# Kernel tuning notes

Hardware: AMD Instinct MI355X
Metric: run time of the kernel (lower is better)

Reference implementation:

```python
import jax, jax.numpy as jnp
import numpy as np

EPS = 1e-05


def setup_inputs() -> dict:
    key = jax.random.key(0)
    kx, kw, kb, kg, kp, kq = jax.random.split(key, 6)
    B, S, D = 32, 1024, 1024
    x = jax.random.normal(kx, (B, S, D), dtype=jnp.float32)
    # Linear(input_size, input_size) params
    W = jax.random.normal(kw, (D, D), dtype=jnp.float32) / np.sqrt(D)
    b = jax.random.normal(kb, (D,), dtype=jnp.float32) * 0.01
    gold_opinion = jax.random.uniform(kg, (B, S, 5), dtype=jnp.float32)
    predict_opinion = jax.random.uniform(kp, (B, S, 5), dtype=jnp.float32)
    gold_prob = jax.random.uniform(kq, (), dtype=jnp.float32)
    return {"x": x, "W": W, "b": b, "gold_opinion": gold_opinion,
            "predict_opinion": predict_opinion, "gold_prob": gold_prob}


def reference(x, W, b, gold_opinion, predict_opinion, gold_prob):
    # x: [B, S, D]
    S = x.shape[-2]
    x_tran = jnp.einsum('bsd,ed->bse', x, W) + b           # Linear: x @ W^T + b
    weights = jnp.einsum('bsd,btd->bst', x_tran, x)        # QK^T -> [B, S, S]

    idx = jnp.arange(S)
    location = jnp.abs(idx[None, :] - idx[:, None]).astype(x.dtype)  # [S, S]
    weights = weights * (1.0 / (location + EPS))           # distance decay

    # use_opinion = True branch
    gold_op = gold_opinion[:, :, 1] + gold_opinion[:, :, 2]          # [B, S]
    pred_op = predict_opinion[:, :, 3] + predict_opinion[:, :, 4]    # [B, S]
    opinion_weights = gold_prob * gold_op + (1.0 - gold_prob) * pred_op
    weights = weights * opinion_weights[:, :, None]

    weights = jnp.exp(jnp.tanh(weights))                   # pseudo-softmax numerator
    off_diag = (location != 0).astype(weights.dtype)       # eye(S) == 0 mask
    weights = weights * off_diag
    weights = weights / (jnp.sum(weights, axis=-1, keepdims=True) + EPS)
    return jnp.einsum('bst,btd->bsd', weights, x)
```

## Files before the change

kernel.cpp:

```cpp
#include <hip/hip_runtime.h>

#define EPSF 1e-5f

typedef _Float16 f16x8 __attribute__((ext_vector_type(8)));
typedef float f32x4 __attribute__((ext_vector_type(4)));

__device__ __forceinline__ void gload_lds16(const _Float16* g, _Float16* l) {
  __builtin_amdgcn_global_load_lds(
      (const __attribute__((address_space(1))) unsigned int*)g,
      (__attribute__((address_space(3))) unsigned int*)l, 16, 0, 0);
}

__device__ __forceinline__ f16x8 cvt8(float4 a, float4 b) {
  f16x8 h;
  h[0] = (_Float16)a.x; h[1] = (_Float16)a.y; h[2] = (_Float16)a.z; h[3] = (_Float16)a.w;
  h[4] = (_Float16)b.x; h[5] = (_Float16)b.y; h[6] = (_Float16)b.z; h[7] = (_Float16)b.w;
  return h;
}

__device__ __forceinline__ void gemm256_run(const _Float16* __restrict__ Ag,
                                            const _Float16* __restrict__ Bg,
                                            _Float16* lds, f32x4 (&acc)[8][4]) {
  const int tid = threadIdx.x;
  const int wave = tid >> 6, lane = tid & 63;
  const int wm = wave >> 2, wn = wave & 3;
  const int quad = lane >> 4, nl = lane & 15;
  const int swz = nl & 7;
  const long stg_off = (long)(wave * 8 + (lane >> 3)) * 1024 +
                       (((lane & 7) ^ (lane >> 3)) * 8);

#pragma unroll
  for (int i = 0; i < 8; ++i)
#pragma unroll
    for (int j = 0; j < 4; ++j) acc[i][j] = (f32x4){0.f, 0.f, 0.f, 0.f};

  f16x8 af[4], bf[4];

#define STG(G, T1, q, isB)                                                   \
  gload_lds16((G) + (long)(q) * 65536 + stg_off + (T1) * 64,                 \
              lds + (((T1) & 1) * 32768 + (isB) * 16384 + (q) * 4096 + wave * 512))
#define LDB4(bb, ksub)                                                       \
  {                                                                          \
    const _Float16* pB_ = lds + (bb) * 32768 + 16384 + (wn * 64 + nl) * 64 + \
                          ((((ksub) * 4 + quad) ^ swz) * 8);                 \
    _Pragma("unroll") for (int j_ = 0; j_ < 4; ++j_)                         \
        bf[j_] = *(const f16x8*)(pB_ + j_ * 1024);                           \
  }
#define LDA4(bb, mq, ksub)                                                   \
  {                                                                          \
    const _Float16* pA_ = lds + (bb) * 32768 +                               \
                          (wm * 128 + (mq) * 64 + nl) * 64 +                 \
                          ((((ksub) * 4 + quad) ^ swz) * 8);                 \
    _Pragma("unroll") for (int i_ = 0; i_ < 4; ++i_)                         \
        af[i_] = *(const f16x8*)(pA_ + i_ * 1024);                           \
  }
#define MFMA16(mq)                                                           \
  {                                                                          \
    __builtin_amdgcn_s_setprio(1);                                           \
    _Pragma("unroll") for (int i_ = 0; i_ < 4; ++i_)                         \
        _Pragma("unroll") for (int j_ = 0; j_ < 4; ++j_)                     \
            acc[(mq) * 4 + i_][j_] = __builtin_amdgcn_mfma_f32_16x16x32_f16( \
                af[i_], bf[j_], acc[(mq) * 4 + i_][j_], 0, 0, 0);            \
    __builtin_amdgcn_s_setprio(0);                                           \
  }
#define BAR __builtin_amdgcn_s_barrier()
#define LGKM0 asm volatile("s_waitcnt lgkmcnt(0)" ::: "memory")
#define VMW2 asm volatile("s_waitcnt vmcnt(2)" ::: "memory")
#define VMW0 asm volatile("s_waitcnt vmcnt(0)" ::: "memory")

  STG(Bg, 0, 0, 1); STG(Bg, 0, 1, 1);
  STG(Ag, 0, 0, 0); STG(Ag, 0, 2, 0);
  STG(Bg, 0, 2, 1); STG(Bg, 0, 3, 1);
  STG(Ag, 0, 1, 0); STG(Ag, 0, 3, 0);
  VMW2;
  BAR;

#pragma unroll 2
  for (int T = 0; T < 15; ++T) {
    const int bb = T & 1;
    LDB4(bb, 0); LDA4(bb, 0, 0);
    STG(Bg, T + 1, 0, 1); STG(Bg, T + 1, 1, 1);
    BAR; LGKM0; MFMA16(0); VMW2; BAR;
    LDA4(bb, 1, 0);
    STG(Ag, T + 1, 0, 0); STG(Ag, T + 1, 2, 0);
    BAR; LGKM0; MFMA16(1); BAR;
    LDB4(bb, 1); LDA4(bb, 0, 1);
    STG(Bg, T + 1, 2, 1); STG(Bg, T + 1, 3, 1);
    BAR; LGKM0; MFMA16(0); BAR;
    LDA4(bb, 1, 1);
    STG(Ag, T + 1, 1, 0); STG(Ag, T + 1, 3, 0);
    BAR; LGKM0; MFMA16(1); VMW2; BAR;
  }
  {
    LDB4(1, 0); LDA4(1, 0, 0);
    BAR; LGKM0; MFMA16(0); VMW0; BAR;
    LDA4(1, 1, 0);
    BAR; LGKM0; MFMA16(1); BAR;
    LDB4(1, 1); LDA4(1, 0, 1);
    BAR; LGKM0; MFMA16(0); BAR;
    LDA4(1, 1, 1);
    BAR; LGKM0; MFMA16(1); BAR;
  }
#undef VMW0
#undef VMW2
#undef LGKM0
#undef BAR
#undef MFMA16
#undef LDA4
#undef LDB4
#undef STG
}

__global__ void prep_opin_k(const float* __restrict__ gold, const float* __restrict__ pred,
                            const float* __restrict__ gprob, float* __restrict__ opin, int n) {
  int i = blockIdx.x * 256 + threadIdx.x;
  if (i >= n) return;
  float gp = gprob[0];
  float go = gold[i * 5 + 1] + gold[i * 5 + 2];
  float po = pred[i * 5 + 3] + pred[i * 5 + 4];
  opin[i] = gp * go + (1.0f - gp) * po;
}

__global__ __launch_bounds__(256) void prep_h_k(const float* __restrict__ src,
                                                _Float16* __restrict__ dst) {
  long i = ((long)blockIdx.x * 256 + threadIdx.x) * 8;
  float4 a = *(const float4*)(src + i);
  float4 b = *(const float4*)(src + i + 4);
  *(f16x8*)(dst + i) = cvt8(a, b);
}

__global__ __launch_bounds__(256) void prep_xt_k(const float* __restrict__ x,
                                                 _Float16* __restrict__ XhT) {
  __shared__ _Float16 T[64][66];
  const int d0 = blockIdx.x * 64, t0 = blockIdx.y * 64;
  const long base = (long)blockIdx.z * 1024;
  const int c = threadIdx.x & 63, tr = threadIdx.x >> 6;
#pragma unroll
  for (int k = 0; k < 16; ++k) {
    int t = k * 4 + tr;
    T[t][c] = (_Float16)x[(base + t0 + t) * 1024 + d0 + c];
  }
  __syncthreads();
#pragma unroll
  for (int k = 0; k < 16; ++k) {
    int d = k * 4 + tr;
    XhT[(base + d0 + d) * 1024 + t0 + c] = T[c][d];
  }
}

__global__ __launch_bounds__(512, 2) void gemm12_k(const _Float16* __restrict__ Xh,
                                                   const _Float16* __restrict__ Wh,
                                                   const float* __restrict__ bias,
                                                   _Float16* __restrict__ XT) {
  __shared__ _Float16 lds[2 * 32768];
  const int lin = blockIdx.x;
  const int ii = lin >> 3;
  const int mt = (lin & 7) * 16 + (ii >> 2);
  const int nt = ii & 3;
  const long m0 = (long)mt * 256;
  const int n0 = nt * 256;

  f32x4 acc[8][4];
  gemm256_run(Xh + m0 * 1024, Wh + (long)n0 * 1024, lds, acc);

  const int tid = threadIdx.x;
  const int wave = tid >> 6, lane = tid & 63;
  const int wm = wave >> 2, wn = wave & 3;
  const int quad = lane >> 4, nl = lane & 15;
#pragma unroll
  for (int mi = 0; mi < 8; ++mi) {
    long gm = m0 + wm * 128 + mi * 16 + quad * 4;
#pragma unroll
    for (int ni = 0; ni < 4; ++ni) {
      int gn = n0 + wn * 64 + ni * 16 + nl;
      float bv = bias[gn];
#pragma unroll
      for (int r = 0; r < 4; ++r)
        XT[(gm + r) * 1024 + gn] = (_Float16)(acc[mi][ni][r] + bv);
    }
  }
}

__global__ __launch_bounds__(512, 2) void scores2_k(const _Float16* __restrict__ XT,
                                                    const _Float16* __restrict__ Xh,
                                                    const float* __restrict__ opin,
                                                    _Float16* __restrict__ P,
                                                    float* __restrict__ denom) {
  __shared__ _Float16 lds[2 * 32768];
  const int lin = blockIdx.x;
  const int ii = lin >> 3;
  const int b = (lin & 7) + 8 * (ii >> 4);
  const int tile = ii & 15;
  const int s0 = (tile >> 2) * 256;
  const int t0 = (tile & 3) * 256;
  const long base = (long)b * 1024;

  f32x4 acc[8][4];
  gemm256_run(XT + (base + s0) * 1024, Xh + (base + t0) * 1024, lds, acc);

  const int tid = threadIdx.x;
  const int wave = tid >> 6, lane = tid & 63;
  const int wm = wave >> 2, wn = wave & 3;
  const int quad = lane >> 4, nl = lane & 15;
#pragma unroll
  for (int mi = 0; mi < 8; ++mi) {
#pragma unroll
    for (int r = 0; r < 4; ++r) {
      int s = s0 + wm * 128 + mi * 16 + quad * 4 + r;
      float opv = opin[b * 1024 + s];
      float rs = 0.f;
#pragma unroll
      for (int ni = 0; ni < 4; ++ni) {
        int tc = t0 + wn * 64 + ni * 16 + nl;
        float loc = fabsf((float)(s - tc));
        float arg = acc[mi][ni][r] * (1.0f / (loc + EPSF)) * opv;
        float th = 1.f - 2.f / (__expf(2.f * arg) + 1.f);
        float p = __expf(th);
        if (s == tc) p = 0.f;
        P[(base + s) * 1024 + tc] = (_Float16)p;
        rs += p;
      }
      rs += __shfl_xor(rs, 1);
      rs += __shfl_xor(rs, 2);
      rs += __shfl_xor(rs, 4);
      rs += __shfl_xor(rs, 8);
      if (nl == 0) atomicAdd(&denom[b * 1024 + s], rs);
    }
  }
}

__global__ __launch_bounds__(512, 2) void pv2_k(const _Float16* __restrict__ P,
                                                const _Float16* __restrict__ XhT,
                                                const float* __restrict__ denom,
                                                float* __restrict__ out) {
  __shared__ _Float16 lds[2 * 32768];
  const int lin = blockIdx.x;
  const int ii = lin >> 3;
  const int b = (lin & 7) + 8 * (ii >> 4);
  const int tile = ii & 15;
  const int s0 = (tile >> 2) * 256;
  const int d0 = (tile & 3) * 256;
  const long base = (long)b * 1024;

  f32x4 acc[8][4];
  gemm256_run(P + (base + s0) * 1024, XhT + (base + d0) * 1024, lds, acc);

  const int tid = threadIdx.x;
  const int wave = tid >> 6, lane = tid & 63;
  const int wm = wave >> 2, wn = wave & 3;
  const int quad = lane >> 4, nl = lane & 15;
#pragma unroll
  for (int mi = 0; mi < 8; ++mi) {
#pragma unroll
    for (int r = 0; r < 4; ++r) {
      int s = s0 + wm * 128 + mi * 16 + quad * 4 + r;
      float inv = 1.0f / (denom[b * 1024 + s] + EPSF);
#pragma unroll
      for (int ni = 0; ni < 4; ++ni) {
        int d = d0 + wn * 64 + ni * 16 + nl;
        out[(base + s) * 1024 + d] = acc[mi][ni][r] * inv;
      }
    }
  }
}

__global__ __launch_bounds__(256) void gemm1_k(const _Float16* __restrict__ Xh,
                                               const float* __restrict__ Wt,
                                               const float* __restrict__ bias,
                                               _Float16* __restrict__ XT) {
  __shared__ _Float16 As[128 * 32];
  __shared__ _Float16 Bs[128 * 32];
  const int tid = threadIdx.x;
  const int wave = tid >> 6, lane = tid & 63;
  const int wm = wave >> 1, wn = wave & 1;
  const int quad = lane >> 4, nl = lane & 15;
  const long m0 = (long)blockIdx.y * 128;
  const int n0 = blockIdx.x * 128;

  f32x4 acc[4][4];
  f32x4 zero = {0.f, 0.f, 0.f, 0.f};
#pragma unroll
  for (int i = 0; i < 4; ++i)
#pragma unroll
    for (int j = 0; j < 4; ++j) acc[i][j] = zero;

  const int crow = tid >> 2;
  const int ckc = (tid & 3) * 8;

  for (int k0 = 0; k0 < 1024; k0 += 32) {
#pragma unroll
    for (int it = 0; it < 2; ++it) {
      int c = it * 256 + tid;
      gload_lds16(Xh + (m0 + (c >> 2)) * 1024 + k0 + (c & 3) * 8,
                  &As[(it * 256 + wave * 64) * 8]);
      int row = it * 64 + crow;
      const float* sb = Wt + (long)(n0 + row) * 1024 + k0 + ckc;
      float4 b0 = *(const float4*)sb;
      float4 b1 = *(const float4*)(sb + 4);
      *(f16x8*)&Bs[row * 32 + ckc] = cvt8(b0, b1);
    }
    __syncthreads();
    f16x8 af[4], bf[4];
#pragma unroll
    for (int mi = 0; mi < 4; ++mi)
      af[mi] = *(const f16x8*)&As[(wm * 64 + mi * 16 + nl) * 32 + quad * 8];
#pragma unroll
    for (int ni = 0; ni < 4; ++ni)
      bf[ni] = *(const f16x8*)&Bs[(wn * 64 + ni * 16 + nl) * 32 + quad * 8];
#pragma unroll
    for (int mi = 0; mi < 4; ++mi)
#pragma unroll
      for (int ni = 0; ni < 4; ++ni)
        acc[mi][ni] = __builtin_amdgcn_mfma_f32_16x16x32_f16(af[mi], bf[ni], acc[mi][ni], 0, 0, 0);
    __syncthreads();
  }

#pragma unroll
  for (int mi = 0; mi < 4; ++mi) {
    long gm = m0 + wm * 64 + mi * 16 + quad * 4;
#pragma unroll
    for (int ni = 0; ni < 4; ++ni) {
      int gn = n0 + wn * 64 + ni * 16 + nl;
      float bv = bias[gn];
#pragma unroll
      for (int r = 0; r < 4; ++r)
        XT[(gm + r) * 1024 + gn] = (_Float16)(acc[mi][ni][r] + bv);
    }
  }
}

__global__ __launch_bounds__(256) void scores_f_k(const _Float16* __restrict__ XT,
                                                  const _Float16* __restrict__ Xh,
                                                  const float* __restrict__ opin,
                                                  _Float16* __restrict__ P,
                                                  float* __restrict__ denom) {
  __shared__ _Float16 As[128 * 32];
  __shared__ _Float16 Bs[128 * 32];
  const int tid = threadIdx.x;
  const int wave = tid >> 6, lane = tid & 63;
  const int wm = wave >> 1, wn = wave & 1;
  const int quad = lane >> 4, nl = lane & 15;
  const int b = blockIdx.z;
  const int s0 = blockIdx.y * 128;
  const int t0 = blockIdx.x * 128;
  const long base = (long)b * 1024;

  f32x4 acc[4][4];
  f32x4 zero = {0.f, 0.f, 0.f, 0.f};
#pragma unroll
  for (int i = 0; i < 4; ++i)
#pragma unroll
    for (int j = 0; j < 4; ++j) acc[i][j] = zero;

  for (int k0 = 0; k0 < 1024; k0 += 32) {
#pragma unroll
    for (int it = 0; it < 2; ++it) {
      int c = it * 256 + tid;
      gload_lds16(XT + (base + s0 + (c >> 2)) * 1024 + k0 + (c & 3) * 8,
                  &As[(it * 256 + wave * 64) * 8]);
      gload_lds16(Xh + (base + t0 + (c >> 2)) * 1024 + k0 + (c & 3) * 8,
                  &Bs[(it * 256 + wave * 64) * 8]);
    }
    __syncthreads();
    f16x8 af[4], bf[4];
#pragma unroll
    for (int mi = 0; mi < 4; ++mi)
      af[mi] = *(const f16x8*)&As[(wm * 64 + mi * 16 + nl) * 32 + quad * 8];
#pragma unroll
    for (int ni = 0; ni < 4; ++ni)
      bf[ni] = *(const f16x8*)&Bs[(wn * 64 + ni * 16 + nl) * 32 + quad * 8];
#pragma unroll
    for (int mi = 0; mi < 4; ++mi)
#pragma unroll
      for (int ni = 0; ni < 4; ++ni)
        acc[mi][ni] = __builtin_amdgcn_mfma_f32_16x16x32_f16(af[mi], bf[ni], acc[mi][ni], 0, 0, 0);
    __syncthreads();
  }

#pragma unroll
  for (int mi = 0; mi < 4; ++mi) {
#pragma unroll
    for (int r = 0; r < 4; ++r) {
      int s = s0 + wm * 64 + mi * 16 + quad * 4 + r;
      float opv = opin[b * 1024 + s];
      float rs = 0.f;
#pragma unroll
      for (int ni = 0; ni < 4; ++ni) {
        int t = t0 + wn * 64 + ni * 16 + nl;
        float loc = fabsf((float)(s - t));
        float arg = acc[mi][ni][r] * (1.0f / (loc + EPSF)) * opv;
        float th = 1.f - 2.f / (__expf(2.f * arg) + 1.f);
        float p = __expf(th);
        if (s == t) p = 0.f;
        P[(base + s) * 1024 + t] = (_Float16)p;
        rs += p;
      }
      rs += __shfl_xor(rs, 1);
      rs += __shfl_xor(rs, 2);
      rs += __shfl_xor(rs, 4);
      rs += __shfl_xor(rs, 8);
      if (nl == 0) atomicAdd(&denom[b * 1024 + s], rs);
    }
  }
}

__global__ __launch_bounds__(256) void pv_k(const _Float16* __restrict__ P,
                                            const float* __restrict__ X,
                                            const float* __restrict__ denom,
                                            float* __restrict__ out) {
  __shared__ _Float16 As[128 * 32];
  __shared__ _Float16 BsT[128 * 40];
  const int tid = threadIdx.x;
  const int wave = tid >> 6, lane = tid & 63;
  const int wm = wave >> 1, wn = wave & 1;
  const int quad = lane >> 4, nl = lane & 15;
  const int b = blockIdx.z;
  const int s0 = blockIdx.y * 128;
  const int d0 = blockIdx.x * 128;
  const long base = (long)b * 1024;

  const int dcol = tid & 127;
  const int tg = tid >> 7;

  f32x4 acc[4][4];
  f32x4 zero = {0.f, 0.f, 0.f, 0.f};
#pragma unroll
  for (int i = 0; i < 4; ++i)
#pragma unroll
    for (int j = 0; j < 4; ++j) acc[i][j] = zero;

  for (int k0 = 0; k0 < 1024; k0 += 32) {
#pragma unroll
    for (int it = 0; it < 2; ++it) {
      int c = it * 256 + tid;
      gload_lds16(P + (base + s0 + (c >> 2)) * 1024 + k0 + (c & 3) * 8,
                  &As[(it * 256 + wave * 64) * 8]);
    }
    {
      const float* xb = X + (base + k0 + tg * 16) * 1024 + d0 + dcol;
      float v[16];
#pragma unroll
      for (int j = 0; j < 16; ++j) v[j] = xb[j * 1024];
      f16x8 h0, h1;
#pragma unroll
      for (int j = 0; j < 8; ++j) { h0[j] = (_Float16)v[j]; h1[j] = (_Float16)v[8 + j]; }
      *(f16x8*)&BsT[dcol * 40 + tg * 16] = h0;
      *(f16x8*)&BsT[dcol * 40 + tg * 16 + 8] = h1;
    }
    __syncthreads();
    f16x8 af[4], bf[4];
#pragma unroll
    for (int mi = 0; mi < 4; ++mi)
      af[mi] = *(const f16x8*)&As[(wm * 64 + mi * 16 + nl) * 32 + quad * 8];
#pragma unroll
    for (int ni = 0; ni < 4; ++ni)
      bf[ni] = *(const f16x8*)&BsT[(wn * 64 + ni * 16 + nl) * 40 + quad * 8];
#pragma unroll
    for (int mi = 0; mi < 4; ++mi)
#pragma unroll
      for (int ni = 0; ni < 4; ++ni)
        acc[mi][ni] = __builtin_amdgcn_mfma_f32_16x16x32_f16(af[mi], bf[ni], acc[mi][ni], 0, 0, 0);
    __syncthreads();
  }

#pragma unroll
  for (int mi = 0; mi < 4; ++mi) {
#pragma unroll
    for (int r = 0; r < 4; ++r) {
      int s = s0 + wm * 64 + mi * 16 + quad * 4 + r;
      float inv = 1.0f / (denom[b * 1024 + s] + EPSF);
#pragma unroll
      for (int ni = 0; ni < 4; ++ni) {
        int d = d0 + wn * 64 + ni * 16 + nl;
        out[(base + s) * 1024 + d] = acc[mi][ni][r] * inv;
      }
    }
  }
}

extern "C" void kernel_launch(void* const* d_in, const int* in_sizes, int n_in,
                              void* d_out, int out_size, void* d_ws, size_t ws_size,
                              hipStream_t stream) {
  (void)in_sizes; (void)n_in; (void)out_size;
  const int B = 32, S = 1024;
  const int BS = B * S;

  const float* x     = (const float*)d_in[0];
  const float* W     = (const float*)d_in[1];
  const float* bias  = (const float*)d_in[2];
  const float* gold  = (const float*)d_in[3];
  const float* pred  = (const float*)d_in[4];
  const float* gprob = (const float*)d_in[5];

  const size_t P_BYTES  = (size_t)BS * 1024 * sizeof(_Float16);
  const size_t XT_BYTES = P_BYTES;
  const size_t OPIN_B   = (size_t)BS * sizeof(float);
  const size_t WH_B     = (size_t)1024 * 1024 * sizeof(_Float16);
  const size_t NEED_BIG = P_BYTES + XT_BYTES + 2 * OPIN_B + WH_B;

  char* ws = (char*)d_ws;
  _Float16* P = (_Float16*)ws;
  const bool big = ws_size >= NEED_BIG;

  _Float16* XT = (_Float16*)d_out;
  _Float16* Xh = XT + (size_t)BS * 1024;
  float* out   = (float*)d_out;

  if (big) {
    _Float16* XhT = (_Float16*)(ws + P_BYTES);
    float* opin   = (float*)(ws + P_BYTES + XT_BYTES);
    float* denom  = opin + BS;
    _Float16* Wh  = (_Float16*)(ws + P_BYTES + XT_BYTES + 2 * OPIN_B);

    hipMemsetAsync(denom, 0, OPIN_B, stream);
    prep_opin_k<<<BS / 256, 256, 0, stream>>>(gold, pred, gprob, opin, BS);
    prep_h_k<<<(BS * 1024 / 8) / 256, 256, 0, stream>>>(x, Xh);
    prep_h_k<<<(1024 * 1024 / 8) / 256, 256, 0, stream>>>(W, Wh);
    prep_xt_k<<<dim3(16, 16, 32), 256, 0, stream>>>(x, XhT);
    gemm12_k<<<512, 512, 0, stream>>>(Xh, Wh, bias, XT);
    scores2_k<<<512, 512, 0, stream>>>(XT, Xh, opin, P, denom);
    pv2_k<<<512, 512, 0, stream>>>(P, XhT, denom, out);
  } else {
    float* opin  = (float*)(ws + P_BYTES);
    float* denom = opin + BS;

    hipMemsetAsync(denom, 0, OPIN_B, stream);
    prep_opin_k<<<BS / 256, 256, 0, stream>>>(gold, pred, gprob, opin, BS);
    prep_h_k<<<(BS * 1024 / 8) / 256, 256, 0, stream>>>(x, Xh);
    gemm1_k<<<dim3(8, 256), 256, 0, stream>>>(Xh, W, bias, XT);
    scores_f_k<<<dim3(8, 8, 32), 256, 0, stream>>>(XT, Xh, opin, P, denom);
    pv_k<<<dim3(8, 8, 32), 256, 0, stream>>>(P, x, denom, out);
  }
}
```

Measured before the change: 513.0 us.

## Fuse x prep kernels, compute opinion in-kernel, replace atomics with partial sums

Merges the fp16 cast and transpose of x into one kernel that reads x once and writes both Xh and XhT. Opinion weights are now computed inside the scores kernel, which drops the separate prep_opin launch and the memset. Row denominators are written as 16 per-slice partials instead of atomicAdds and summed in pv2. The change also adds sched_barrier fences around the MFMA blocks in the GEMM loop and uses hardware v_rcp in the epilogues. In exchange it needs a larger partials workspace, and the approximate reciprocal slightly changes numerics.

```diff
diff --git a/kernel.cpp b/kernel.cpp
--- a/kernel.cpp
+++ b/kernel.cpp
@@ -16,6 +16,12 @@
   h[0] = (_Float16)a.x; h[1] = (_Float16)a.y; h[2] = (_Float16)a.z; h[3] = (_Float16)a.w;
   h[4] = (_Float16)b.x; h[5] = (_Float16)b.y; h[6] = (_Float16)b.z; h[7] = (_Float16)b.w;
   return h;
+}
+
+__device__ __forceinline__ float frcp(float x) {
+  float r;
+  asm("v_rcp_f32 %0, %1" : "=v"(r) : "v"(x));
+  return r;
 }
 
 __device__ __forceinline__ void gemm256_run(const _Float16* __restrict__ Ag,
@@ -64,6 +70,7 @@
     __builtin_amdgcn_s_setprio(0);                                           \
   }
 #define BAR __builtin_amdgcn_s_barrier()
+#define SCHED0 __builtin_amdgcn_sched_barrier(0)
 #define LGKM0 asm volatile("s_waitcnt lgkmcnt(0)" ::: "memory")
 #define VMW2 asm volatile("s_waitcnt vmcnt(2)" ::: "memory")
 #define VMW0 asm volatile("s_waitcnt vmcnt(0)" ::: "memory")
@@ -80,30 +87,31 @@
     const int bb = T & 1;
     LDB4(bb, 0); LDA4(bb, 0, 0);
     STG(Bg, T + 1, 0, 1); STG(Bg, T + 1, 1, 1);
-    BAR; LGKM0; MFMA16(0); VMW2; BAR;
+    SCHED0; BAR; LGKM0; SCHED0; MFMA16(0); VMW2; BAR;
     LDA4(bb, 1, 0);
     STG(Ag, T + 1, 0, 0); STG(Ag, T + 1, 2, 0);
-    BAR; LGKM0; MFMA16(1); BAR;
+    SCHED0; BAR; LGKM0; SCHED0; MFMA16(1); BAR;
     LDB4(bb, 1); LDA4(bb, 0, 1);
     STG(Bg, T + 1, 2, 1); STG(Bg, T + 1, 3, 1);
-    BAR; LGKM0; MFMA16(0); BAR;
+    SCHED0; BAR; LGKM0; SCHED0; MFMA16(0); BAR;
     LDA4(bb, 1, 1);
     STG(Ag, T + 1, 1, 0); STG(Ag, T + 1, 3, 0);
-    BAR; LGKM0; MFMA16(1); VMW2; BAR;
+    SCHED0; BAR; LGKM0; SCHED0; MFMA16(1); VMW2; BAR;
   }
   {
     LDB4(1, 0); LDA4(1, 0, 0);
-    BAR; LGKM0; MFMA16(0); VMW0; BAR;
+    SCHED0; BAR; LGKM0; SCHED0; MFMA16(0); VMW0; BAR;
     LDA4(1, 1, 0);
-    BAR; LGKM0; MFMA16(1); BAR;
+    SCHED0; BAR; LGKM0; SCHED0; MFMA16(1); BAR;
     LDB4(1, 1); LDA4(1, 0, 1);
-    BAR; LGKM0; MFMA16(0); BAR;
+    SCHED0; BAR; LGKM0; SCHED0; MFMA16(0); BAR;
     LDA4(1, 1, 1);
-    BAR; LGKM0; MFMA16(1); BAR;
+    SCHED0; BAR; LGKM0; SCHED0; MFMA16(1); BAR;
   }
 #undef VMW0
 #undef VMW2
 #undef LGKM0
+#undef SCHED0
 #undef BAR
 #undef MFMA16
 #undef LDA4
@@ -129,8 +137,9 @@
   *(f16x8*)(dst + i) = cvt8(a, b);
 }
 
-__global__ __launch_bounds__(256) void prep_xt_k(const float* __restrict__ x,
-                                                 _Float16* __restrict__ XhT) {
+__global__ __launch_bounds__(256) void prep_x_k(const float* __restrict__ x,
+                                                _Float16* __restrict__ Xh,
+                                                _Float16* __restrict__ XhT) {
   __shared__ _Float16 T[64][66];
   const int d0 = blockIdx.x * 64, t0 = blockIdx.y * 64;
   const long base = (long)blockIdx.z * 1024;
@@ -138,7 +147,10 @@
 #pragma unroll
   for (int k = 0; k < 16; ++k) {
     int t = k * 4 + tr;
-    T[t][c] = (_Float16)x[(base + t0 + t) * 1024 + d0 + c];
+    float v = x[(base + t0 + t) * 1024 + d0 + c];
+    _Float16 h = (_Float16)v;
+    Xh[(base + t0 + t) * 1024 + d0 + c] = h;
+    T[t][c] = h;
   }
   __syncthreads();
 #pragma unroll
@@ -183,9 +195,11 @@
 
 __global__ __launch_bounds__(512, 2) void scores2_k(const _Float16* __restrict__ XT,
                                                     const _Float16* __restrict__ Xh,
-                                                    const float* __restrict__ opin,
+                                                    const float* __restrict__ gold,
+                                                    const float* __restrict__ pred,
+                                                    const float* __restrict__ gprob,
                                                     _Float16* __restrict__ P,
-                                                    float* __restrict__ denom) {
+                                                    float* __restrict__ dpart) {
   __shared__ _Float16 lds[2 * 32768];
   const int lin = blockIdx.x;
   const int ii = lin >> 3;
@@ -199,22 +213,35 @@
   gemm256_run(XT + (base + s0) * 1024, Xh + (base + t0) * 1024, lds, acc);
 
   const int tid = threadIdx.x;
+  float* sop = (float*)lds;
+  if (tid < 256) {
+    int s = s0 + tid;
+    float gp = gprob[0];
+    long o = (base + s) * 5;
+    float go = gold[o + 1] + gold[o + 2];
+    float po = pred[o + 3] + pred[o + 4];
+    sop[tid] = gp * go + (1.0f - gp) * po;
+  }
+  __syncthreads();
+
   const int wave = tid >> 6, lane = tid & 63;
   const int wm = wave >> 2, wn = wave & 3;
   const int quad = lane >> 4, nl = lane & 15;
+  const int slice = (tile & 3) * 4 + wn;
 #pragma unroll
   for (int mi = 0; mi < 8; ++mi) {
 #pragma unroll
     for (int r = 0; r < 4; ++r) {
-      int s = s0 + wm * 128 + mi * 16 + quad * 4 + r;
-      float opv = opin[b * 1024 + s];
+      int sl = wm * 128 + mi * 16 + quad * 4 + r;
+      int s = s0 + sl;
+      float opv = sop[sl];
       float rs = 0.f;
 #pragma unroll
       for (int ni = 0; ni < 4; ++ni) {
         int tc = t0 + wn * 64 + ni * 16 + nl;
         float loc = fabsf((float)(s - tc));
-        float arg = acc[mi][ni][r] * (1.0f / (loc + EPSF)) * opv;
-        float th = 1.f - 2.f / (__expf(2.f * arg) + 1.f);
+        float arg = acc[mi][ni][r] * frcp(loc + EPSF) * opv;
+        float th = 1.f - 2.f * frcp(__expf(2.f * arg) + 1.f);
         float p = __expf(th);
         if (s == tc) p = 0.f;
         P[(base + s) * 1024 + tc] = (_Float16)p;
@@ -224,14 +251,14 @@
       rs += __shfl_xor(rs, 2);
       rs += __shfl_xor(rs, 4);
       rs += __shfl_xor(rs, 8);
-      if (nl == 0) atomicAdd(&denom[b * 1024 + s], rs);
+      if (nl == 0) dpart[(((long)slice * 32 + b) << 10) + s] = rs;
     }
   }
 }
 
 __global__ __launch_bounds__(512, 2) void pv2_k(const _Float16* __restrict__ P,
                                                 const _Float16* __restrict__ XhT,
-                                                const float* __restrict__ denom,
+                                                const float* __restrict__ dpart,
                                                 float* __restrict__ out) {
   __shared__ _Float16 lds[2 * 32768];
   const int lin = blockIdx.x;
@@ -246,6 +273,16 @@
   gemm256_run(P + (base + s0) * 1024, XhT + (base + d0) * 1024, lds, acc);
 
   const int tid = threadIdx.x;
+  float* sden = (float*)lds;
+  if (tid < 256) {
+    float sum = 0.f;
+#pragma unroll
+    for (int k = 0; k < 16; ++k)
+      sum += dpart[(((long)k * 32 + b) << 10) + s0 + tid];
+    sden[tid] = frcp(sum + EPSF);
+  }
+  __syncthreads();
+
   const int wave = tid >> 6, lane = tid & 63;
   const int wm = wave >> 2, wn = wave & 3;
   const int quad = lane >> 4, nl = lane & 15;
@@ -253,8 +290,9 @@
   for (int mi = 0; mi < 8; ++mi) {
 #pragma unroll
     for (int r = 0; r < 4; ++r) {
-      int s = s0 + wm * 128 + mi * 16 + quad * 4 + r;
-      float inv = 1.0f / (denom[b * 1024 + s] + EPSF);
+      int sl = wm * 128 + mi * 16 + quad * 4 + r;
+      int s = s0 + sl;
+      float inv = sden[sl];
 #pragma unroll
       for (int ni = 0; ni < 4; ++ni) {
         int d = d0 + wn * 64 + ni * 16 + nl;
@@ -494,9 +532,10 @@
 
   const size_t P_BYTES  = (size_t)BS * 1024 * sizeof(_Float16);
   const size_t XT_BYTES = P_BYTES;
+  const size_t DP_B     = (size_t)16 * BS * sizeof(float);
+  const size_t WH_B     = (size_t)1024 * 1024 * sizeof(_Float16);
   const size_t OPIN_B   = (size_t)BS * sizeof(float);
-  const size_t WH_B     = (size_t)1024 * 1024 * sizeof(_Float16);
-  const size_t NEED_BIG = P_BYTES + XT_BYTES + 2 * OPIN_B + WH_B;
+  const size_t NEED_BIG = P_BYTES + XT_BYTES + DP_B + WH_B;
 
   char* ws = (char*)d_ws;
   _Float16* P = (_Float16*)ws;
@@ -508,18 +547,14 @@
 
   if (big) {
     _Float16* XhT = (_Float16*)(ws + P_BYTES);
-    float* opin   = (float*)(ws + P_BYTES + XT_BYTES);
-    float* denom  = opin + BS;
-    _Float16* Wh  = (_Float16*)(ws + P_BYTES + XT_BYTES + 2 * OPIN_B);
-
-    hipMemsetAsync(denom, 0, OPIN_B, stream);
-    prep_opin_k<<<BS / 256, 256, 0, stream>>>(gold, pred, gprob, opin, BS);
-    prep_h_k<<<(BS * 1024 / 8) / 256, 256, 0, stream>>>(x, Xh);
+    float* dpart  = (float*)(ws + P_BYTES + XT_BYTES);
+    _Float16* Wh  = (_Float16*)(ws + P_BYTES + XT_BYTES + DP_B);
+
+    prep_x_k<<<dim3(16, 16, 32), 256, 0, stream>>>(x, Xh, XhT);
     prep_h_k<<<(1024 * 1024 / 8) / 256, 256, 0, stream>>>(W, Wh);
-    prep_xt_k<<<dim3(16, 16, 32), 256, 0, stream>>>(x, XhT);
     gemm12_k<<<512, 512, 0, stream>>>(Xh, Wh, bias, XT);
-    scores2_k<<<512, 512, 0, stream>>>(XT, Xh, opin, P, denom);
-    pv2_k<<<512, 512, 0, stream>>>(P, XhT, denom, out);
+    scores2_k<<<512, 512, 0, stream>>>(XT, Xh, gold, pred, gprob, P, dpart);
+    pv2_k<<<512, 512, 0, stream>>>(P, XhT, dpart, out);
   } else {
     float* opin  = (float*)(ws + P_BYTES);
     float* denom = opin + BS;
```

Measured after the change: 489.5 us. 4.6% less time.
